# Kernel optimization log

Hardware: AMD Instinct MI355X
Metric: run time of the kernel (lower is better)

The kernel has to match this reference:

```python
import jax, jax.numpy as jnp
import numpy as np

D = 2048          # lstm_size
V = 4096          # uniform num_tokens for all 5 decision groups
NUM_LAYERS = 4    # len(num_tokens) - 1 loop iterations; one final decode after


def setup_inputs() -> dict:
    key = jax.random.key(0)
    ks = jax.random.split(key, 10)
    s = 0.02
    n = lambda k, shape: jax.random.normal(k, shape, dtype=jnp.float32) * s
    return {
        "emb0": n(ks[0], (1, D)),                 # Embedding(1, D) initial input
        "w_ih": n(ks[1], (4 * D, D)),             # LSTMCell input weights (i,f,g,o)
        "w_hh": n(ks[2], (4 * D, D)),
        "b_ih": jnp.zeros((4 * D,), jnp.float32),
        "b_hh": jnp.zeros((4 * D,), jnp.float32),
        "lin1_w": n(ks[3], (D, D)),
        "lin1_b": jnp.zeros((D,), jnp.float32),
        "lin2_w": n(ks[4], (D, D)),
        "lin2_b": jnp.zeros((D,), jnp.float32),
        "lin3_w": n(ks[5], (1, D)),
        "lin3_b": jnp.zeros((1,), jnp.float32),
        "dec_w": n(ks[6], (5, V, D)),             # 5 decoders Linear(D, V)
        "dec_b": jnp.zeros((5, V), jnp.float32),
        "emb_tables": n(ks[7], (4, V, D)),        # only embeddings[0..3] are used
    }


def _lstm_cell(x, h, c, w_ih, w_hh, b_ih, b_hh):
    # torch.nn.LSTMCell math; gate order i, f, g, o
    gates = x @ w_ih.T + b_ih + h @ w_hh.T + b_hh
    i, f, g, o = jnp.split(gates, 4, axis=-1)
    i, f, o = jax.nn.sigmoid(i), jax.nn.sigmoid(f), jax.nn.sigmoid(o)
    g = jnp.tanh(g)
    c_new = f * c + i * g
    h_new = o * jnp.tanh(c_new)
    return h_new, c_new


def reference(emb0, w_ih, w_hh, b_ih, b_hh, lin1_w, lin1_b, lin2_w, lin2_b,
              lin3_w, lin3_b, dec_w, dec_b, emb_tables):
    key = jax.random.key(42)
    step = 0

    def sample(logits, step):
        # stable softmax stats computed once via log_softmax
        logp = jax.nn.log_softmax(logits, axis=-1)
        p = jnp.exp(logp)
        ent = -(logp * p).sum(1)                              # (1,)
        idx = jax.random.categorical(jax.random.fold_in(key, step), logits, axis=-1)  # (1,)
        sel_lp = jnp.take_along_axis(logp, idx[:, None], axis=1).squeeze(1)           # (1,)
        return idx, sel_lp, jax.lax.stop_gradient(ent)

    # NOTE: source names the LSTMCell outputs (next_c, next_h) = lstm(...),
    # i.e. swapped vs torch's (h, c). State threading stays consistent, but all
    # downstream linears/decoders/all_h consume the CELL state c. Reproduced here.
    h = jnp.zeros((1, D), jnp.float32)
    c = jnp.zeros((1, D), jnp.float32)
    inputs = emb0
    all_c, all_cw = [], []
    arc, lps, ents = [], [], []

    for layer_id in range(NUM_LAYERS):
        h, c = _lstm_cell(inputs, h, c, w_ih, w_hh, b_ih, b_hh)
        all_c.append(c)
        all_cw.append(c @ lin1_w.T + lin1_b)
        query = jnp.tanh((c @ lin2_w.T + lin2_b) + jnp.concatenate(all_cw, 0))  # (layer_id+1, D)
        logits = (query @ lin3_w.T + lin3_b).reshape(1, layer_id + 1)
        skip_idx, lp, en = sample(logits, step); step += 1
        arc.append(skip_idx); lps.append(lp); ents.append(en)
        inputs = jnp.concatenate(all_c, 0)[skip_idx]            # (1, D)

        h, c = _lstm_cell(inputs, h, c, w_ih, w_hh, b_ih, b_hh)
        logits = c @ dec_w[layer_id].T + dec_b[layer_id]        # (1, V)
        func, lp, en = sample(logits, step); step += 1
        arc.append(func); lps.append(lp); ents.append(en)
        inputs = emb_tables[layer_id][func]                     # (1, D)

    # final model decision
    h, c = _lstm_cell(inputs, h, c, w_ih, w_hh, b_ih, b_hh)
    logits = c @ dec_w[-1].T + dec_b[-1]
    func, lp, en = sample(logits, step)
    arc.append(func); lps.append(lp); ents.append(en)

    arc_seq = jnp.concatenate(arc, 0)            # (9,) int32
    sample_entropy = jnp.concatenate(ents, 0)    # (9,)
    sample_log_probs = jnp.concatenate(lps, 0)   # (9,)
    return arc_seq, sample_entropy, sample_log_probs
```

## Files before the change

kernel.cpp:

```cpp
#include <hip/hip_runtime.h>
#include <stdint.h>

#define D 2048
#define V 4096
#define TINYF 1.17549435e-38f
#define NINF (-__builtin_huge_valf())

#if __has_builtin(__builtin_amdgcn_cvt_pk_f32_fp8) && __has_builtin(__builtin_amdgcn_cvt_pk_fp8_f32)
#define HWFP8 1
#define POSTSCALE 0.015625f
#else
#define HWFP8 0
#define POSTSCALE 1.52587890625e-05f
#endif

typedef float vfloat2 __attribute__((ext_vector_type(2)));
typedef float vfloat4 __attribute__((ext_vector_type(4)));

__device__ __forceinline__ void tf_block(uint32_t k0, uint32_t k1, uint32_t x0, uint32_t x1,
                                         uint32_t& o0, uint32_t& o1) {
  uint32_t ks2 = k0 ^ k1 ^ 0x1BD11BDAu;
  uint32_t ks[3] = {k0, k1, ks2};
  x0 += k0; x1 += k1;
  const uint32_t rotA[4] = {13u, 15u, 26u, 6u};
  const uint32_t rotB[4] = {17u, 29u, 16u, 24u};
#pragma unroll
  for (int i = 0; i < 5; ++i) {
    const uint32_t* rot = (i & 1) ? rotB : rotA;
#pragma unroll
    for (int j = 0; j < 4; ++j) {
      uint32_t r = rot[j];
      x0 += x1;
      x1 = (x1 << r) | (x1 >> (32u - r));
      x1 ^= x0;
    }
    x0 += ks[(i + 1) % 3];
    x1 += ks[(i + 2) % 3] + (uint32_t)(i + 1);
  }
  o0 = x0; o1 = x1;
}

__device__ __forceinline__ float gumbel_at(uint32_t k1, uint32_t k2, int i) {
  uint32_t o0, o1;
  tf_block(k1, k2, 0u, (uint32_t)i, o0, o1);
  uint32_t bits = o0 ^ o1;
  float u = __uint_as_float((bits >> 9) | 0x3F800000u) - 1.0f;
  u = fmaxf(TINYF, u + TINYF);
  return -logf(-logf(u));
}

#if !HWFP8
__device__ __forceinline__ float dec1(uint32_t v) {
  uint32_t e = (v >> 3) & 15u, m = v & 7u;
  int K = e ? (int)((8u + m) << e) : (int)(m << 1);
  float f = (float)K;
  return (v & 0x80u) ? -f : f;
}
__device__ __forceinline__ uint32_t enc1(float xf) {
  uint32_t b = __float_as_uint(xf);
  uint32_t s = (b >> 24) & 0x80u;
  float ax = fabsf(xf);
  if (ax < 0.015625f) return s | (uint32_t)(int)rintf(ax * 512.f);
  uint32_t ab = b & 0x7FFFFFFFu;
  ab += 0x7FFFFu + ((ab >> 20) & 1u);
  int e = (int)(ab >> 23) - 120;
  uint32_t m = (ab >> 20) & 7u;
  if (e < 1) return s | (uint32_t)(int)rintf(ax * 512.f);
  if (e > 15) { e = 15; m = 7u; }
  return s | ((uint32_t)e << 3) | m;
}
#endif

__device__ __forceinline__ void dec8(uint2 u, float* w) {
#if HWFP8
  vfloat2 a = __builtin_amdgcn_cvt_pk_f32_fp8((int)u.x, false);
  vfloat2 b = __builtin_amdgcn_cvt_pk_f32_fp8((int)u.x, true);
  vfloat2 c = __builtin_amdgcn_cvt_pk_f32_fp8((int)u.y, false);
  vfloat2 d = __builtin_amdgcn_cvt_pk_f32_fp8((int)u.y, true);
  w[0] = a.x; w[1] = a.y; w[2] = b.x; w[3] = b.y;
  w[4] = c.x; w[5] = c.y; w[6] = d.x; w[7] = d.y;
#else
  uint32_t p = u.x, q = u.y;
  w[0] = dec1(p & 255u); w[1] = dec1((p >> 8) & 255u);
  w[2] = dec1((p >> 16) & 255u); w[3] = dec1(p >> 24);
  w[4] = dec1(q & 255u); w[5] = dec1((q >> 8) & 255u);
  w[6] = dec1((q >> 16) & 255u); w[7] = dec1(q >> 24);
#endif
}

__device__ __forceinline__ uint2 enc8(const float* v) {
  uint2 o;
#if HWFP8
  int lo = __builtin_amdgcn_cvt_pk_fp8_f32(v[0], v[1], 0, false);
  lo     = __builtin_amdgcn_cvt_pk_fp8_f32(v[2], v[3], lo, true);
  int hi = __builtin_amdgcn_cvt_pk_fp8_f32(v[4], v[5], 0, false);
  hi     = __builtin_amdgcn_cvt_pk_fp8_f32(v[6], v[7], hi, true);
  o.x = (uint32_t)lo; o.y = (uint32_t)hi;
#else
  o.x = enc1(v[0]) | (enc1(v[1]) << 8) | (enc1(v[2]) << 16) | (enc1(v[3]) << 24);
  o.y = enc1(v[4]) | (enc1(v[5]) << 8) | (enc1(v[6]) << 16) | (enc1(v[7]) << 24);
#endif
  return o;
}

__device__ __forceinline__ float4 ntload4(const float4* p) {
  vfloat4 v = __builtin_nontemporal_load((const vfloat4*)p);
  return make_float4(v.x, v.y, v.z, v.w);
}

__device__ __forceinline__ float row_dot8(const uint8_t* __restrict__ row,
                                          const float* __restrict__ xs, int lane) {
  float a = 0.f;
#pragma unroll
  for (int k = lane * 8; k < D; k += 512) {
    uint2 u = *(const uint2*)(row + k);
    float w[8]; dec8(u, w);
    float4 x0 = *(const float4*)(xs + k);
    float4 x1 = *(const float4*)(xs + k + 4);
    a += w[0] * x0.x + w[1] * x0.y + w[2] * x0.z + w[3] * x0.w
       + w[4] * x1.x + w[5] * x1.y + w[6] * x1.z + w[7] * x1.w;
  }
  return a;
}

__device__ __forceinline__ float row_dot_conv(const float* __restrict__ row,
                                              const float* __restrict__ xs, int lane,
                                              uint8_t* __restrict__ out8) {
  float a = 0.f;
#pragma unroll
  for (int k = lane * 8; k < D; k += 512) {
    float4 w0 = ntload4((const float4*)(row + k));
    float4 w1 = ntload4((const float4*)(row + k + 4));
    float4 x0 = *(const float4*)(xs + k);
    float4 x1 = *(const float4*)(xs + k + 4);
    a += w0.x * x0.x + w0.y * x0.y + w0.z * x0.z + w0.w * x0.w
       + w1.x * x1.x + w1.y * x1.y + w1.z * x1.z + w1.w * x1.w;
    float v[8] = {w0.x * 64.f, w0.y * 64.f, w0.z * 64.f, w0.w * 64.f,
                  w1.x * 64.f, w1.y * 64.f, w1.z * 64.f, w1.w * 64.f};
    *(uint2*)(out8 + k) = enc8(v);
  }
  return a;
}

struct SampPart { float m, S, T, bv; int bi; };

__device__ __forceinline__ void merge_part(SampPart& a, float qm, float qS, float qT,
                                           float qb, int qi) {
  float nm = fmaxf(a.m, qm);
  float ea = expf(a.m - nm), eq = expf(qm - nm);
  a.T = (a.T + (a.m - nm) * a.S) * ea + (qT + (qm - nm) * qS) * eq;
  a.S = a.S * ea + qS * eq;
  a.m = nm;
  if (qb > a.bv || (qb == a.bv && qi < a.bi)) { a.bv = qb; a.bi = qi; }
}

__device__ __forceinline__ SampPart reduce_parts(const float4* __restrict__ part4,
                                                 const int* __restrict__ parti,
                                                 float* rm, float* rS, float* rT,
                                                 float* rb, int* ri, int tid) {
  float4 p = part4[4 * tid];
  SampPart a = {p.x, p.y, p.z, p.w, parti[4 * tid]};
#pragma unroll
  for (int r = 1; r < 4; ++r) {
    float4 q = part4[4 * tid + r];
    merge_part(a, q.x, q.y, q.z, q.w, parti[4 * tid + r]);
  }
  rm[tid] = a.m; rS[tid] = a.S; rT[tid] = a.T; rb[tid] = a.bv; ri[tid] = a.bi;
  __syncthreads();
  for (int st = 128; st; st >>= 1) {
    if (tid < st) {
      merge_part(a, rm[tid + st], rS[tid + st], rT[tid + st], rb[tid + st], ri[tid + st]);
      rm[tid] = a.m; rS[tid] = a.S; rT[tid] = a.T; rb[tid] = a.bv; ri[tid] = a.bi;
    }
    __syncthreads();
  }
  SampPart res = {rm[0], rS[0], rT[0], rb[0], ri[0]};
  __syncthreads();
  return res;
}

__device__ __forceinline__ void block_partial(const float* sl4, int base, int step,
                                              float4* __restrict__ part4,
                                              int* __restrict__ parti, int blk) {
  uint32_t k1, k2; tf_block(0u, 42u, 0u, (uint32_t)step, k1, k2);
  float x0 = sl4[0], x1 = sl4[1], x2 = sl4[2], x3 = sl4[3];
  float pm = fmaxf(fmaxf(x0, x1), fmaxf(x2, x3));
  float e0 = expf(x0 - pm), e1 = expf(x1 - pm), e2 = expf(x2 - pm), e3 = expf(x3 - pm);
  float pS = e0 + e1 + e2 + e3;
  float pT = e0 * (x0 - pm) + e1 * (x1 - pm) + e2 * (x2 - pm) + e3 * (x3 - pm);
  float pb = NINF; int pbi = base;
  float g;
  g = gumbel_at(k1, k2, base + 0) + x0; if (g > pb) { pb = g; pbi = base + 0; }
  g = gumbel_at(k1, k2, base + 1) + x1; if (g > pb) { pb = g; pbi = base + 1; }
  g = gumbel_at(k1, k2, base + 2) + x2; if (g > pb) { pb = g; pbi = base + 2; }
  g = gumbel_at(k1, k2, base + 3) + x3; if (g > pb) { pb = g; pbi = base + 3; }
  part4[blk] = make_float4(pm, pS, pT, pb);
  parti[blk] = pbi;
}

template <bool CONV, bool SAMPLE>
__global__ __launch_bounds__(256) void lstm_cell_k(
    const void* __restrict__ w_ih_v, const void* __restrict__ w_hh_v,
    uint8_t* __restrict__ wih8_out, uint8_t* __restrict__ whh8_out,
    const float* __restrict__ b_ih, const float* __restrict__ b_hh,
    const float* __restrict__ x_base,
    const float4* __restrict__ part4, const int* __restrict__ parti,
    const float* __restrict__ logits,
    const float* __restrict__ h_in, const float* __restrict__ c_in,
    float* __restrict__ h_out, float* __restrict__ c_out, float* __restrict__ c_copy,
    float* __restrict__ out_arc, float* __restrict__ out_ent, float* __restrict__ out_lp) {
  __shared__ float xs[D];
  __shared__ float hs[D];
  __shared__ float rm[256], rS[256], rT[256], rb[256];
  __shared__ int ri[256];
  int tid = threadIdx.x;
  const float* x = x_base;
  if (SAMPLE) {
    SampPart g = reduce_parts(part4, parti, rm, rS, rT, rb, ri, tid);
    if (tid == 0 && blockIdx.x == 0) {
      float L = logf(g.S);
      *out_arc = (float)g.bi;
      *out_ent = L - g.T / g.S;
      *out_lp  = logits[g.bi] - g.m - L;
    }
    x = x_base + (size_t)g.bi * D;
  }
  for (int i = tid; i < D; i += 256) { xs[i] = x[i]; hs[i] = h_in ? h_in[i] : 0.f; }
  __syncthreads();
  int wave = tid >> 6, lane = tid & 63;
  int j = blockIdx.x * 4 + wave;
  float gv[4];
#pragma unroll
  for (int m4 = 0; m4 < 4; ++m4) {
    size_t roff = (size_t)(m4 * D + j) * D;
    float a;
    if (CONV) {
      a = row_dot_conv((const float*)w_ih_v + roff, xs, lane, wih8_out + roff)
        + row_dot_conv((const float*)w_hh_v + roff, hs, lane, whh8_out + roff);
    } else {
      a = row_dot8((const uint8_t*)w_ih_v + roff, xs, lane)
        + row_dot8((const uint8_t*)w_hh_v + roff, hs, lane);
      a *= POSTSCALE;
    }
#pragma unroll
    for (int off = 32; off > 0; off >>= 1) a += __shfl_down(a, off, 64);
    gv[m4] = a + b_ih[m4 * D + j] + b_hh[m4 * D + j];
  }
  if (lane == 0) {
    float ig = 1.f / (1.f + expf(-gv[0]));
    float fg = 1.f / (1.f + expf(-gv[1]));
    float gg = tanhf(gv[2]);
    float og = 1.f / (1.f + expf(-gv[3]));
    float ci = c_in ? c_in[j] : 0.f;
    float cn = fg * ci + ig * gg;
    float hn = og * tanhf(cn);
    c_out[j] = cn;
    h_out[j] = hn;
    if (c_copy) c_copy[j] = cn;
  }
}

template <int NC, bool CONV>
__global__ __launch_bounds__(256) void spec_lin_k(
    const uint8_t* __restrict__ w_ih, const uint8_t* __restrict__ w_hh,
    const float* __restrict__ b_ih, const float* __restrict__ b_hh,
    const float* __restrict__ h1, const float* __restrict__ all_c,
    const void* __restrict__ l1_v, const float* __restrict__ l1b,
    const void* __restrict__ l2_v, const float* __restrict__ l2b,
    uint8_t* __restrict__ l18_out, uint8_t* __restrict__ l28_out,
    const float* __restrict__ c1,
    float* __restrict__ g_ih, float* __restrict__ g_hh,
    float* __restrict__ cw_dst, float* __restrict__ qb) {
  __shared__ float xs[D];
  int tid = threadIdx.x;
  int wave = tid >> 6, lane = tid & 63;
  int b = blockIdx.x;
  if (b < 512) {
    int j = b * 4 + wave;
    float acc[4][NC + 1];
#pragma unroll
    for (int m = 0; m < 4; ++m)
#pragma unroll
      for (int t = 0; t < NC + 1; ++t) acc[m][t] = 0.f;
    for (int k = lane * 8; k < D; k += 512) {
      float xh[8];
      float xc[NC][8];
      *(float4*)xh       = *(const float4*)(h1 + k);
      *(float4*)(xh + 4) = *(const float4*)(h1 + k + 4);
#pragma unroll
      for (int t = 0; t < NC; ++t) {
        *(float4*)(xc[t])     = *(const float4*)(all_c + (size_t)t * D + k);
        *(float4*)(xc[t] + 4) = *(const float4*)(all_c + (size_t)t * D + k + 4);
      }
#pragma unroll
      for (int m = 0; m < 4; ++m) {
        float wi[8], wh[8];
        dec8(*(const uint2*)(w_ih + (size_t)(m * D + j) * D + k), wi);
        dec8(*(const uint2*)(w_hh + (size_t)(m * D + j) * D + k), wh);
#pragma unroll
        for (int e = 0; e < 8; ++e) acc[m][0] += wh[e] * xh[e];
#pragma unroll
        for (int t = 0; t < NC; ++t)
#pragma unroll
          for (int e = 0; e < 8; ++e) acc[m][1 + t] += wi[e] * xc[t][e];
      }
    }
#pragma unroll
    for (int m = 0; m < 4; ++m)
#pragma unroll
      for (int t = 0; t < NC + 1; ++t) {
        float a = acc[m][t];
#pragma unroll
        for (int o = 32; o > 0; o >>= 1) a += __shfl_down(a, o, 64);
        if (lane == 0) {
          if (t == 0) g_hh[m * D + j] = a * POSTSCALE + b_ih[m * D + j] + b_hh[m * D + j];
          else        g_ih[((size_t)(t - 1) * 4 + m) * D + j] = a * POSTSCALE;
        }
      }
  } else {
    for (int i = tid; i < D; i += 256) xs[i] = c1[i];
    __syncthreads();
    int b2 = b - 512;
    const void* Wp; const float* bp; float* dst; uint8_t* o8; int row;
    if (b2 < 512) { row = b2 * 4 + wave; Wp = l1_v; bp = l1b; dst = cw_dst; o8 = l18_out; }
    else          { row = (b2 - 512) * 4 + wave; Wp = l2_v; bp = l2b; dst = qb; o8 = l28_out; }
    size_t roff = (size_t)row * D;
    float a;
    if (CONV) a = row_dot_conv((const float*)Wp + roff, xs, lane, o8 + roff);
    else      a = row_dot8((const uint8_t*)Wp + roff, xs, lane) * POSTSCALE;
#pragma unroll
    for (int o = 32; o > 0; o >>= 1) a += __shfl_down(a, o, 64);
    if (lane == 0) dst[row] = a + bp[row];
  }
}

__global__ __launch_bounds__(256) void dec_fused_k(
    const float* __restrict__ Wdec, const float* __restrict__ bdec,
    const float* __restrict__ g_ih, const float* __restrict__ g_hh,
    const float* __restrict__ c1,
    const float* __restrict__ qb, const float* __restrict__ all_cw,
    const float* __restrict__ lin3_w, const float* __restrict__ lin3_b,
    int ncand, int step,
    float* __restrict__ logits,
    float* __restrict__ h2_out, float* __restrict__ c2_out,
    float* __restrict__ out_arc, float* __restrict__ out_ent, float* __restrict__ out_lp,
    float4* __restrict__ part4, int* __restrict__ parti) {
  __shared__ float xs[D];
  __shared__ float red[16];
  __shared__ float sl4[4];
  __shared__ int s_sel;
  int tid = threadIdx.x, wave = tid >> 6, lane = tid & 63;
  for (int t = 0; t < ncand; ++t) {
    float s = 0.f;
    for (int k = tid; k < D; k += 256) s += tanhf(qb[k] + all_cw[(size_t)t * D + k]) * lin3_w[k];
#pragma unroll
    for (int o = 32; o > 0; o >>= 1) s += __shfl_down(s, o, 64);
    if (lane == 0) red[t * 4 + wave] = s;
  }
  __syncthreads();
  if (tid == 0) {
    float sl[4];
    for (int t = 0; t < ncand; ++t)
      sl[t] = red[t * 4] + red[t * 4 + 1] + red[t * 4 + 2] + red[t * 4 + 3] + lin3_b[0];
    uint32_t k1, k2; tf_block(0u, 42u, 0u, (uint32_t)step, k1, k2);
    float m = NINF;
    for (int i = 0; i < ncand; ++i) m = fmaxf(m, sl[i]);
    float S = 0.f, T = 0.f;
    for (int i = 0; i < ncand; ++i) { float e = expf(sl[i] - m); S += e; T += e * (sl[i] - m); }
    float L = logf(S);
    float bv = NINF; int bi = 0;
    for (int i = 0; i < ncand; ++i) {
      float sc = gumbel_at(k1, k2, i) + sl[i];
      if (sc > bv) { bv = sc; bi = i; }
    }
    s_sel = bi;
    if (blockIdx.x == 0) {
      *out_arc = (float)bi;
      *out_ent = L - T / S;
      *out_lp  = sl[bi] - m - L;
    }
  }
  __syncthreads();
  int sel = s_sel;
  const float* gi = g_ih + (size_t)sel * 4 * D;
  bool b0 = (blockIdx.x == 0);
  for (int j = tid; j < D; j += 256) {
    float gI = gi[j]         + g_hh[j];
    float gF = gi[D + j]     + g_hh[D + j];
    float gG = gi[2 * D + j] + g_hh[2 * D + j];
    float gO = gi[3 * D + j] + g_hh[3 * D + j];
    float ig = 1.f / (1.f + expf(-gI));
    float fg = 1.f / (1.f + expf(-gF));
    float gg = tanhf(gG);
    float og = 1.f / (1.f + expf(-gO));
    float cn = fg * c1[j] + ig * gg;
    xs[j] = cn;
    if (b0) { c2_out[j] = cn; h2_out[j] = og * tanhf(cn); }
  }
  __syncthreads();
  int row = blockIdx.x * 4 + wave;
  const float* wr = Wdec + (size_t)row * D;
  float a = 0.f;
#pragma unroll
  for (int k = lane * 4; k < D; k += 256) {
    float4 w = ntload4((const float4*)(wr + k));
    float4 x = *(const float4*)(xs + k);
    a += w.x * x.x + w.y * x.y + w.z * x.z + w.w * x.w;
  }
#pragma unroll
  for (int o = 32; o > 0; o >>= 1) a += __shfl_down(a, o, 64);
  if (lane == 0) { float lv = a + bdec[row]; logits[row] = lv; sl4[wave] = lv; }
  __syncthreads();
  if (tid == 0) block_partial(sl4, blockIdx.x * 4, step + 1, part4, parti, blockIdx.x);
}

__global__ __launch_bounds__(256) void gemv_k(
    const float* __restrict__ W, const float* __restrict__ bias,
    const float* __restrict__ c, float* __restrict__ y, int step,
    float4* __restrict__ part4, int* __restrict__ parti) {
  __shared__ float xs[D];
  __shared__ float sl4[4];
  int tid = threadIdx.x;
  for (int i = tid; i < D; i += 256) xs[i] = c[i];
  __syncthreads();
  int wave = tid >> 6, lane = tid & 63;
  int row = blockIdx.x * 4 + wave;
  const float* wr = W + (size_t)row * D;
  float a = 0.f;
#pragma unroll
  for (int k = lane * 4; k < D; k += 256) {
    float4 w = ntload4((const float4*)(wr + k));
    float4 x = *(const float4*)(xs + k);
    a += w.x * x.x + w.y * x.y + w.z * x.z + w.w * x.w;
  }
#pragma unroll
  for (int o = 32; o > 0; o >>= 1) a += __shfl_down(a, o, 64);
  if (lane == 0) { float lv = a + bias[row]; y[row] = lv; sl4[wave] = lv; }
  __syncthreads();
  if (tid == 0) block_partial(sl4, blockIdx.x * 4, step, part4, parti, blockIdx.x);
}

__global__ __launch_bounds__(256) void reduce_sample_k(
    const float4* __restrict__ part4, const int* __restrict__ parti,
    const float* __restrict__ logits,
    float* __restrict__ out_arc, float* __restrict__ out_ent, float* __restrict__ out_lp) {
  __shared__ float rm[256], rS[256], rT[256], rb[256];
  __shared__ int ri[256];
  int tid = threadIdx.x;
  SampPart g = reduce_parts(part4, parti, rm, rS, rT, rb, ri, tid);
  if (tid == 0) {
    float L = logf(g.S);
    *out_arc = (float)g.bi;
    *out_ent = L - g.T / g.S;
    *out_lp  = logits[g.bi] - g.m - L;
  }
}

extern "C" void kernel_launch(void* const* d_in, const int* in_sizes, int n_in,
                              void* d_out, int out_size, void* d_ws, size_t ws_size,
                              hipStream_t stream) {
  const float* emb0   = (const float*)d_in[0];
  const float* w_ih   = (const float*)d_in[1];
  const float* w_hh   = (const float*)d_in[2];
  const float* b_ih   = (const float*)d_in[3];
  const float* b_hh   = (const float*)d_in[4];
  const float* lin1_w = (const float*)d_in[5];
  const float* lin1_b = (const float*)d_in[6];
  const float* lin2_w = (const float*)d_in[7];
  const float* lin2_b = (const float*)d_in[8];
  const float* lin3_w = (const float*)d_in[9];
  const float* lin3_b = (const float*)d_in[10];
  const float* dec_w  = (const float*)d_in[11];
  const float* dec_b  = (const float*)d_in[12];
  const float* embt   = (const float*)d_in[13];

  float* out = (float*)d_out;
  float* ws = (float*)d_ws;

  float* hA     = ws;
  float* cA     = ws + D;
  float* hB     = ws + 2 * D;
  float* cB     = ws + 3 * D;
  float* all_c  = ws + 4 * D;
  float* all_cw = ws + 8 * D;
  float* qb     = ws + 12 * D;
  float* logits = ws + 13 * D;
  float* g_hh   = ws + 15 * D;
  float* g_ih   = ws + 19 * D;
  float4* part4 = (float4*)(ws + 36 * D);
  int* parti    = (int*)(ws + 38 * D);
  uint8_t* w8   = (uint8_t*)(ws + 40 * D);
  uint8_t* wih8 = w8;
  uint8_t* whh8 = w8 + (size_t)4 * D * D;
  uint8_t* l18  = w8 + (size_t)8 * D * D;
  uint8_t* l28  = w8 + (size_t)9 * D * D;

  for (int layer = 0; layer < 4; ++layer) {
    float* ccopy = all_c + (size_t)layer * D;
    if (layer == 0) {
      lstm_cell_k<true, false><<<512, 256, 0, stream>>>(
          w_ih, w_hh, wih8, whh8, b_ih, b_hh, emb0,
          nullptr, nullptr, nullptr, nullptr, nullptr,
          hA, cA, ccopy, nullptr, nullptr, nullptr);
    } else {
      int ps = 2 * layer - 1;
      lstm_cell_k<false, true><<<512, 256, 0, stream>>>(
          wih8, whh8, nullptr, nullptr, b_ih, b_hh,
          embt + (size_t)(layer - 1) * V * D,
          part4, parti, logits, hB, cB,
          hA, cA, ccopy, out + ps, out + 9 + ps, out + 18 + ps);
    }
    float* cw = all_cw + (size_t)layer * D;
    if (layer == 0) {
      spec_lin_k<1, true><<<1536, 256, 0, stream>>>(
          wih8, whh8, b_ih, b_hh, hA, all_c,
          lin1_w, lin1_b, lin2_w, lin2_b, l18, l28,
          cA, g_ih, g_hh, cw, qb);
    } else {
      switch (layer) {
        case 1:  spec_lin_k<2, false><<<1536, 256, 0, stream>>>(wih8, whh8, b_ih, b_hh, hA, all_c, l18, lin1_b, l28, lin2_b, nullptr, nullptr, cA, g_ih, g_hh, cw, qb); break;
        case 2:  spec_lin_k<3, false><<<1536, 256, 0, stream>>>(wih8, whh8, b_ih, b_hh, hA, all_c, l18, lin1_b, l28, lin2_b, nullptr, nullptr, cA, g_ih, g_hh, cw, qb); break;
        default: spec_lin_k<4, false><<<1536, 256, 0, stream>>>(wih8, whh8, b_ih, b_hh, hA, all_c, l18, lin1_b, l28, lin2_b, nullptr, nullptr, cA, g_ih, g_hh, cw, qb); break;
      }
    }
    int step = 2 * layer;
    dec_fused_k<<<V / 4, 256, 0, stream>>>(dec_w + (size_t)layer * V * D,
                                           dec_b + (size_t)layer * V,
                                           g_ih, g_hh, cA, qb, all_cw, lin3_w, lin3_b,
                                           layer + 1, step, logits, hB, cB,
                                           out + step, out + 9 + step, out + 18 + step,
                                           part4, parti);
  }

  lstm_cell_k<false, true><<<512, 256, 0, stream>>>(
      wih8, whh8, nullptr, nullptr, b_ih, b_hh,
      embt + (size_t)3 * V * D, part4, parti, logits, hB, cB,
      hA, cA, nullptr, out + 7, out + 16, out + 25);
  gemv_k<<<V / 4, 256, 0, stream>>>(dec_w + (size_t)4 * V * D, dec_b + (size_t)4 * V,
                                    cA, logits, 8, part4, parti);
  reduce_sample_k<<<1, 256, 0, stream>>>(part4, parti, logits, out + 8, out + 17, out + 26);
}
```

Baseline: 265.8 us.

## Skip zero-state W_hh in first LSTM cell, interleave gate loads, prefetch decoder rows

The first LSTM cell no longer multiplies by W_hh, since the initial hidden state is zero. The fp32-to-fp8 conversion of W_hh moves into the speculative linear kernel, which already reads that matrix. The LSTM and linear GEMV loops now interleave all four gate rows per k step, so more loads are in flight at once. The decoder and final GEMV kernels load their weight rows into registers before the dependent sampling and LSTM work, hiding memory latency behind the serial phase. The cost is higher register pressure, and the first speculative kernel now reads fp32 W_hh.

```diff
diff --git a/kernel.cpp b/kernel.cpp
--- a/kernel.cpp
+++ b/kernel.cpp
@@ -106,40 +106,6 @@
 __device__ __forceinline__ float4 ntload4(const float4* p) {
   vfloat4 v = __builtin_nontemporal_load((const vfloat4*)p);
   return make_float4(v.x, v.y, v.z, v.w);
-}
-
-__device__ __forceinline__ float row_dot8(const uint8_t* __restrict__ row,
-                                          const float* __restrict__ xs, int lane) {
-  float a = 0.f;
-#pragma unroll
-  for (int k = lane * 8; k < D; k += 512) {
-    uint2 u = *(const uint2*)(row + k);
-    float w[8]; dec8(u, w);
-    float4 x0 = *(const float4*)(xs + k);
-    float4 x1 = *(const float4*)(xs + k + 4);
-    a += w[0] * x0.x + w[1] * x0.y + w[2] * x0.z + w[3] * x0.w
-       + w[4] * x1.x + w[5] * x1.y + w[6] * x1.z + w[7] * x1.w;
-  }
-  return a;
-}
-
-__device__ __forceinline__ float row_dot_conv(const float* __restrict__ row,
-                                              const float* __restrict__ xs, int lane,
-                                              uint8_t* __restrict__ out8) {
-  float a = 0.f;
-#pragma unroll
-  for (int k = lane * 8; k < D; k += 512) {
-    float4 w0 = ntload4((const float4*)(row + k));
-    float4 w1 = ntload4((const float4*)(row + k + 4));
-    float4 x0 = *(const float4*)(xs + k);
-    float4 x1 = *(const float4*)(xs + k + 4);
-    a += w0.x * x0.x + w0.y * x0.y + w0.z * x0.z + w0.w * x0.w
-       + w1.x * x1.x + w1.y * x1.y + w1.z * x1.z + w1.w * x1.w;
-    float v[8] = {w0.x * 64.f, w0.y * 64.f, w0.z * 64.f, w0.w * 64.f,
-                  w1.x * 64.f, w1.y * 64.f, w1.z * 64.f, w1.w * 64.f};
-    *(uint2*)(out8 + k) = enc8(v);
-  }
-  return a;
 }
 
 struct SampPart { float m, S, T, bv; int bi; };
@@ -201,7 +167,7 @@
 template <bool CONV, bool SAMPLE>
 __global__ __launch_bounds__(256) void lstm_cell_k(
     const void* __restrict__ w_ih_v, const void* __restrict__ w_hh_v,
-    uint8_t* __restrict__ wih8_out, uint8_t* __restrict__ whh8_out,
+    uint8_t* __restrict__ wih8_out,
     const float* __restrict__ b_ih, const float* __restrict__ b_hh,
     const float* __restrict__ x_base,
     const float4* __restrict__ part4, const int* __restrict__ parti,
@@ -225,33 +191,60 @@
     }
     x = x_base + (size_t)g.bi * D;
   }
-  for (int i = tid; i < D; i += 256) { xs[i] = x[i]; hs[i] = h_in ? h_in[i] : 0.f; }
+  for (int i = tid; i < D; i += 256) {
+    xs[i] = x[i];
+    if (!CONV) hs[i] = h_in[i];
+  }
   __syncthreads();
   int wave = tid >> 6, lane = tid & 63;
   int j = blockIdx.x * 4 + wave;
+  float accI[4] = {0.f, 0.f, 0.f, 0.f};
+  float accH[4] = {0.f, 0.f, 0.f, 0.f};
+  for (int k = lane * 8; k < D; k += 512) {
+    float x8[8];
+    *(float4*)x8       = *(const float4*)(xs + k);
+    *(float4*)(x8 + 4) = *(const float4*)(xs + k + 4);
+    float h8[8];
+    if (!CONV) {
+      *(float4*)h8       = *(const float4*)(hs + k);
+      *(float4*)(h8 + 4) = *(const float4*)(hs + k + 4);
+    }
+#pragma unroll
+    for (int m = 0; m < 4; ++m) {
+      size_t roff = (size_t)(m * D + j) * D + k;
+      if (CONV) {
+        float4 w0 = ntload4((const float4*)((const float*)w_ih_v + roff));
+        float4 w1 = ntload4((const float4*)((const float*)w_ih_v + roff + 4));
+        accI[m] += w0.x * x8[0] + w0.y * x8[1] + w0.z * x8[2] + w0.w * x8[3]
+                 + w1.x * x8[4] + w1.y * x8[5] + w1.z * x8[6] + w1.w * x8[7];
+        float v[8] = {w0.x * 64.f, w0.y * 64.f, w0.z * 64.f, w0.w * 64.f,
+                      w1.x * 64.f, w1.y * 64.f, w1.z * 64.f, w1.w * 64.f};
+        *(uint2*)(wih8_out + roff) = enc8(v);
+      } else {
+        float wi[8], wh[8];
+        dec8(*(const uint2*)((const uint8_t*)w_ih_v + roff), wi);
+        dec8(*(const uint2*)((const uint8_t*)w_hh_v + roff), wh);
+#pragma unroll
+        for (int e = 0; e < 8; ++e) accI[m] += wi[e] * x8[e];
+#pragma unroll
+        for (int e = 0; e < 8; ++e) accH[m] += wh[e] * h8[e];
+      }
+    }
+  }
   float gv[4];
 #pragma unroll
-  for (int m4 = 0; m4 < 4; ++m4) {
-    size_t roff = (size_t)(m4 * D + j) * D;
-    float a;
-    if (CONV) {
-      a = row_dot_conv((const float*)w_ih_v + roff, xs, lane, wih8_out + roff)
-        + row_dot_conv((const float*)w_hh_v + roff, hs, lane, whh8_out + roff);
-    } else {
-      a = row_dot8((const uint8_t*)w_ih_v + roff, xs, lane)
-        + row_dot8((const uint8_t*)w_hh_v + roff, hs, lane);
-      a *= POSTSCALE;
-    }
+  for (int m = 0; m < 4; ++m) {
+    float a = CONV ? accI[m] : (accI[m] + accH[m]) * POSTSCALE;
 #pragma unroll
     for (int off = 32; off > 0; off >>= 1) a += __shfl_down(a, off, 64);
-    gv[m4] = a + b_ih[m4 * D + j] + b_hh[m4 * D + j];
+    gv[m] = a + b_ih[m * D + j] + b_hh[m * D + j];
   }
   if (lane == 0) {
     float ig = 1.f / (1.f + expf(-gv[0]));
     float fg = 1.f / (1.f + expf(-gv[1]));
     float gg = tanhf(gv[2]);
     float og = 1.f / (1.f + expf(-gv[3]));
-    float ci = c_in ? c_in[j] : 0.f;
+    float ci = CONV ? 0.f : c_in[j];
     float cn = fg * ci + ig * gg;
     float hn = og * tanhf(cn);
     c_out[j] = cn;
@@ -262,7 +255,8 @@
 
 template <int NC, bool CONV>
 __global__ __launch_bounds__(256) void spec_lin_k(
-    const uint8_t* __restrict__ w_ih, const uint8_t* __restrict__ w_hh,
+    const uint8_t* __restrict__ wih8, const void* __restrict__ whh_v,
+    uint8_t* __restrict__ whh8_out,
     const float* __restrict__ b_ih, const float* __restrict__ b_hh,
     const float* __restrict__ h1, const float* __restrict__ all_c,
     const void* __restrict__ l1_v, const float* __restrict__ l1b,
@@ -294,9 +288,20 @@
       }
 #pragma unroll
       for (int m = 0; m < 4; ++m) {
+        size_t roff = (size_t)(m * D + j) * D + k;
         float wi[8], wh[8];
-        dec8(*(const uint2*)(w_ih + (size_t)(m * D + j) * D + k), wi);
-        dec8(*(const uint2*)(w_hh + (size_t)(m * D + j) * D + k), wh);
+        dec8(*(const uint2*)(wih8 + roff), wi);
+        if (CONV) {
+          float4 w0 = ntload4((const float4*)((const float*)whh_v + roff));
+          float4 w1 = ntload4((const float4*)((const float*)whh_v + roff + 4));
+          wh[0] = w0.x; wh[1] = w0.y; wh[2] = w0.z; wh[3] = w0.w;
+          wh[4] = w1.x; wh[5] = w1.y; wh[6] = w1.z; wh[7] = w1.w;
+          float v[8] = {w0.x * 64.f, w0.y * 64.f, w0.z * 64.f, w0.w * 64.f,
+                        w1.x * 64.f, w1.y * 64.f, w1.z * 64.f, w1.w * 64.f};
+          *(uint2*)(whh8_out + roff) = enc8(v);
+        } else {
+          dec8(*(const uint2*)((const uint8_t*)whh_v + roff), wh);
+        }
 #pragma unroll
         for (int e = 0; e < 8; ++e) acc[m][0] += wh[e] * xh[e];
 #pragma unroll
@@ -313,8 +318,12 @@
 #pragma unroll
         for (int o = 32; o > 0; o >>= 1) a += __shfl_down(a, o, 64);
         if (lane == 0) {
-          if (t == 0) g_hh[m * D + j] = a * POSTSCALE + b_ih[m * D + j] + b_hh[m * D + j];
-          else        g_ih[((size_t)(t - 1) * 4 + m) * D + j] = a * POSTSCALE;
+          if (t == 0) {
+            float sc = CONV ? 1.f : POSTSCALE;
+            g_hh[m * D + j] = a * sc + b_ih[m * D + j] + b_hh[m * D + j];
+          } else {
+            g_ih[((size_t)(t - 1) * 4 + m) * D + j] = a * POSTSCALE;
+          }
         }
       }
   } else {
@@ -324,10 +333,28 @@
     const void* Wp; const float* bp; float* dst; uint8_t* o8; int row;
     if (b2 < 512) { row = b2 * 4 + wave; Wp = l1_v; bp = l1b; dst = cw_dst; o8 = l18_out; }
     else          { row = (b2 - 512) * 4 + wave; Wp = l2_v; bp = l2b; dst = qb; o8 = l28_out; }
-    size_t roff = (size_t)row * D;
-    float a;
-    if (CONV) a = row_dot_conv((const float*)Wp + roff, xs, lane, o8 + roff);
-    else      a = row_dot8((const uint8_t*)Wp + roff, xs, lane) * POSTSCALE;
+    size_t rbase = (size_t)row * D;
+    float a = 0.f;
+    for (int k = lane * 8; k < D; k += 512) {
+      float x0[8];
+      *(float4*)x0       = *(const float4*)(xs + k);
+      *(float4*)(x0 + 4) = *(const float4*)(xs + k + 4);
+      if (CONV) {
+        float4 w0 = ntload4((const float4*)((const float*)Wp + rbase + k));
+        float4 w1 = ntload4((const float4*)((const float*)Wp + rbase + k + 4));
+        a += w0.x * x0[0] + w0.y * x0[1] + w0.z * x0[2] + w0.w * x0[3]
+           + w1.x * x0[4] + w1.y * x0[5] + w1.z * x0[6] + w1.w * x0[7];
+        float v[8] = {w0.x * 64.f, w0.y * 64.f, w0.z * 64.f, w0.w * 64.f,
+                      w1.x * 64.f, w1.y * 64.f, w1.z * 64.f, w1.w * 64.f};
+        *(uint2*)(o8 + rbase + k) = enc8(v);
+      } else {
+        float w[8];
+        dec8(*(const uint2*)((const uint8_t*)Wp + rbase + k), w);
+#pragma unroll
+        for (int e = 0; e < 8; ++e) a += w[e] * x0[e];
+      }
+    }
+    if (!CONV) a *= POSTSCALE;
 #pragma unroll
     for (int o = 32; o > 0; o >>= 1) a += __shfl_down(a, o, 64);
     if (lane == 0) dst[row] = a + bp[row];
@@ -350,6 +377,12 @@
   __shared__ float sl4[4];
   __shared__ int s_sel;
   int tid = threadIdx.x, wave = tid >> 6, lane = tid & 63;
+  int row = blockIdx.x * 4 + wave;
+  const float* wr = Wdec + (size_t)row * D;
+  float4 wreg[8];
+#pragma unroll
+  for (int kk = 0; kk < 8; ++kk)
+    wreg[kk] = ntload4((const float4*)(wr + lane * 4 + kk * 256));
   for (int t = 0; t < ncand; ++t) {
     float s = 0.f;
     for (int k = tid; k < D; k += 256) s += tanhf(qb[k] + all_cw[(size_t)t * D + k]) * lin3_w[k];
@@ -398,14 +431,11 @@
     if (b0) { c2_out[j] = cn; h2_out[j] = og * tanhf(cn); }
   }
   __syncthreads();
-  int row = blockIdx.x * 4 + wave;
-  const float* wr = Wdec + (size_t)row * D;
   float a = 0.f;
 #pragma unroll
-  for (int k = lane * 4; k < D; k += 256) {
-    float4 w = ntload4((const float4*)(wr + k));
-    float4 x = *(const float4*)(xs + k);
-    a += w.x * x.x + w.y * x.y + w.z * x.z + w.w * x.w;
+  for (int kk = 0; kk < 8; ++kk) {
+    float4 x = *(const float4*)(xs + lane * 4 + kk * 256);
+    a += wreg[kk].x * x.x + wreg[kk].y * x.y + wreg[kk].z * x.z + wreg[kk].w * x.w;
   }
 #pragma unroll
   for (int o = 32; o > 0; o >>= 1) a += __shfl_down(a, o, 64);
@@ -420,18 +450,20 @@
     float4* __restrict__ part4, int* __restrict__ parti) {
   __shared__ float xs[D];
   __shared__ float sl4[4];
-  int tid = threadIdx.x;
-  for (int i = tid; i < D; i += 256) xs[i] = c[i];
-  __syncthreads();
-  int wave = tid >> 6, lane = tid & 63;
+  int tid = threadIdx.x, wave = tid >> 6, lane = tid & 63;
   int row = blockIdx.x * 4 + wave;
   const float* wr = W + (size_t)row * D;
+  float4 wreg[8];
+#pragma unroll
+  for (int kk = 0; kk < 8; ++kk)
+    wreg[kk] = ntload4((const float4*)(wr + lane * 4 + kk * 256));
+  for (int i = tid; i < D; i += 256) xs[i] = c[i];
+  __syncthreads();
   float a = 0.f;
 #pragma unroll
-  for (int k = lane * 4; k < D; k += 256) {
-    float4 w = ntload4((const float4*)(wr + k));
-    float4 x = *(const float4*)(xs + k);
-    a += w.x * x.x + w.y * x.y + w.z * x.z + w.w * x.w;
+  for (int kk = 0; kk < 8; ++kk) {
+    float4 x = *(const float4*)(xs + lane * 4 + kk * 256);
+    a += wreg[kk].x * x.x + wreg[kk].y * x.y + wreg[kk].z * x.z + wreg[kk].w * x.w;
   }
 #pragma unroll
   for (int o = 32; o > 0; o >>= 1) a += __shfl_down(a, o, 64);
@@ -499,13 +531,13 @@
     float* ccopy = all_c + (size_t)layer * D;
     if (layer == 0) {
       lstm_cell_k<true, false><<<512, 256, 0, stream>>>(
-          w_ih, w_hh, wih8, whh8, b_ih, b_hh, emb0,
+          w_ih, nullptr, wih8, b_ih, b_hh, emb0,
           nullptr, nullptr, nullptr, nullptr, nullptr,
           hA, cA, ccopy, nullptr, nullptr, nullptr);
     } else {
       int ps = 2 * layer - 1;
       lstm_cell_k<false, true><<<512, 256, 0, stream>>>(
-          wih8, whh8, nullptr, nullptr, b_ih, b_hh,
+          wih8, whh8, nullptr, b_ih, b_hh,
           embt + (size_t)(layer - 1) * V * D,
           part4, parti, logits, hB, cB,
           hA, cA, ccopy, out + ps, out + 9 + ps, out + 18 + ps);
@@ -513,14 +545,14 @@
     float* cw = all_cw + (size_t)layer * D;
     if (layer == 0) {
       spec_lin_k<1, true><<<1536, 256, 0, stream>>>(
-          wih8, whh8, b_ih, b_hh, hA, all_c,
+          wih8, w_hh, whh8, b_ih, b_hh, hA, all_c,
           lin1_w, lin1_b, lin2_w, lin2_b, l18, l28,
           cA, g_ih, g_hh, cw, qb);
     } else {
       switch (layer) {
-        case 1:  spec_lin_k<2, false><<<1536, 256, 0, stream>>>(wih8, whh8, b_ih, b_hh, hA, all_c, l18, lin1_b, l28, lin2_b, nullptr, nullptr, cA, g_ih, g_hh, cw, qb); break;
-        case 2:  spec_lin_k<3, false><<<1536, 256, 0, stream>>>(wih8, whh8, b_ih, b_hh, hA, all_c, l18, lin1_b, l28, lin2_b, nullptr, nullptr, cA, g_ih, g_hh, cw, qb); break;
-        default: spec_lin_k<4, false><<<1536, 256, 0, stream>>>(wih8, whh8, b_ih, b_hh, hA, all_c, l18, lin1_b, l28, lin2_b, nullptr, nullptr, cA, g_ih, g_hh, cw, qb); break;
+        case 1:  spec_lin_k<2, false><<<1536, 256, 0, stream>>>(wih8, whh8, nullptr, b_ih, b_hh, hA, all_c, l18, lin1_b, l28, lin2_b, nullptr, nullptr, cA, g_ih, g_hh, cw, qb); break;
+        case 2:  spec_lin_k<3, false><<<1536, 256, 0, stream>>>(wih8, whh8, nullptr, b_ih, b_hh, hA, all_c, l18, lin1_b, l28, lin2_b, nullptr, nullptr, cA, g_ih, g_hh, cw, qb); break;
+        default: spec_lin_k<4, false><<<1536, 256, 0, stream>>>(wih8, whh8, nullptr, b_ih, b_hh, hA, all_c, l18, lin1_b, l28, lin2_b, nullptr, nullptr, cA, g_ih, g_hh, cw, qb); break;
       }
     }
     int step = 2 * layer;
@@ -533,7 +565,7 @@
   }
 
   lstm_cell_k<false, true><<<512, 256, 0, stream>>>(
-      wih8, whh8, nullptr, nullptr, b_ih, b_hh,
+      wih8, whh8, nullptr, b_ih, b_hh,
       embt + (size_t)3 * V * D, part4, parti, logits, hB, cB,
       hA, cA, nullptr, out + 7, out + 16, out + 25);
   gemv_k<<<V / 4, 256, 0, stream>>>(dec_w + (size_t)4 * V * D, dec_b + (size_t)4 * V,
```

Result: slower. 271.6 us (+2.2%).

## Split LSTM cell work so each block owns one hidden unit across four gate waves

Applied to the files above, without the earlier changes.

The LSTM cell kernel now launches one block per hidden unit (2048 blocks), with each of the four waves computing one gate row. Previously each wave computed all four gate rows serially across 512 blocks. The gate results are combined through shared memory before thread 0 applies the cell update. The sampling reduction scratch now aliases the xs shared buffer to cut shared memory use, and the fp8 dot product is inlined with separate ih/hh accumulators. Each block still redundantly reduces the sampling partials and loads x/h into shared memory, so that per-block overhead is now paid four times as often.

```diff
diff --git a/kernel.cpp b/kernel.cpp
--- a/kernel.cpp
+++ b/kernel.cpp
@@ -211,11 +211,15 @@
     float* __restrict__ out_arc, float* __restrict__ out_ent, float* __restrict__ out_lp) {
   __shared__ float xs[D];
   __shared__ float hs[D];
-  __shared__ float rm[256], rS[256], rT[256], rb[256];
-  __shared__ int ri[256];
+  __shared__ float sgv[4];
   int tid = threadIdx.x;
   const float* x = x_base;
   if (SAMPLE) {
+    float* rm = xs;
+    float* rS = xs + 256;
+    float* rT = xs + 512;
+    float* rb = xs + 768;
+    int*   ri = (int*)(xs + 1024);
     SampPart g = reduce_parts(part4, parti, rm, rS, rT, rb, ri, tid);
     if (tid == 0 && blockIdx.x == 0) {
       float L = logf(g.S);
@@ -225,32 +229,50 @@
     }
     x = x_base + (size_t)g.bi * D;
   }
-  for (int i = tid; i < D; i += 256) { xs[i] = x[i]; hs[i] = h_in ? h_in[i] : 0.f; }
+  for (int i = tid; i < D; i += 256) {
+    xs[i] = x[i];
+    hs[i] = h_in ? h_in[i] : 0.f;
+  }
   __syncthreads();
   int wave = tid >> 6, lane = tid & 63;
-  int j = blockIdx.x * 4 + wave;
-  float gv[4];
-#pragma unroll
-  for (int m4 = 0; m4 < 4; ++m4) {
-    size_t roff = (size_t)(m4 * D + j) * D;
-    float a;
-    if (CONV) {
-      a = row_dot_conv((const float*)w_ih_v + roff, xs, lane, wih8_out + roff)
-        + row_dot_conv((const float*)w_hh_v + roff, hs, lane, whh8_out + roff);
-    } else {
-      a = row_dot8((const uint8_t*)w_ih_v + roff, xs, lane)
-        + row_dot8((const uint8_t*)w_hh_v + roff, hs, lane);
-      a *= POSTSCALE;
-    }
-#pragma unroll
-    for (int off = 32; off > 0; off >>= 1) a += __shfl_down(a, off, 64);
-    gv[m4] = a + b_ih[m4 * D + j] + b_hh[m4 * D + j];
-  }
-  if (lane == 0) {
-    float ig = 1.f / (1.f + expf(-gv[0]));
-    float fg = 1.f / (1.f + expf(-gv[1]));
-    float gg = tanhf(gv[2]);
-    float og = 1.f / (1.f + expf(-gv[3]));
+  int j = blockIdx.x;
+  int m = wave;
+  size_t roff = (size_t)(m * D + j) * D;
+  float a;
+  if (CONV) {
+    a = row_dot_conv((const float*)w_ih_v + roff, xs, lane, wih8_out + roff)
+      + row_dot_conv((const float*)w_hh_v + roff, hs, lane, whh8_out + roff);
+  } else {
+    const uint8_t* ri8 = (const uint8_t*)w_ih_v + roff;
+    const uint8_t* rh8 = (const uint8_t*)w_hh_v + roff;
+    float accI = 0.f, accH = 0.f;
+#pragma unroll
+    for (int k = lane * 8; k < D; k += 512) {
+      uint2 ui = *(const uint2*)(ri8 + k);
+      uint2 uh = *(const uint2*)(rh8 + k);
+      float wi[8], wh[8];
+      dec8(ui, wi);
+      dec8(uh, wh);
+      float4 x0 = *(const float4*)(xs + k);
+      float4 x1 = *(const float4*)(xs + k + 4);
+      float4 h0 = *(const float4*)(hs + k);
+      float4 h1 = *(const float4*)(hs + k + 4);
+      accI += wi[0] * x0.x + wi[1] * x0.y + wi[2] * x0.z + wi[3] * x0.w
+            + wi[4] * x1.x + wi[5] * x1.y + wi[6] * x1.z + wi[7] * x1.w;
+      accH += wh[0] * h0.x + wh[1] * h0.y + wh[2] * h0.z + wh[3] * h0.w
+            + wh[4] * h1.x + wh[5] * h1.y + wh[6] * h1.z + wh[7] * h1.w;
+    }
+    a = (accI + accH) * POSTSCALE;
+  }
+#pragma unroll
+  for (int off = 32; off > 0; off >>= 1) a += __shfl_down(a, off, 64);
+  if (lane == 0) sgv[m] = a + b_ih[m * D + j] + b_hh[m * D + j];
+  __syncthreads();
+  if (tid == 0) {
+    float ig = 1.f / (1.f + expf(-sgv[0]));
+    float fg = 1.f / (1.f + expf(-sgv[1]));
+    float gg = tanhf(sgv[2]);
+    float og = 1.f / (1.f + expf(-sgv[3]));
     float ci = c_in ? c_in[j] : 0.f;
     float cn = fg * ci + ig * gg;
     float hn = og * tanhf(cn);
@@ -294,9 +316,10 @@
       }
 #pragma unroll
       for (int m = 0; m < 4; ++m) {
+        size_t roff = (size_t)(m * D + j) * D + k;
         float wi[8], wh[8];
-        dec8(*(const uint2*)(w_ih + (size_t)(m * D + j) * D + k), wi);
-        dec8(*(const uint2*)(w_hh + (size_t)(m * D + j) * D + k), wh);
+        dec8(*(const uint2*)(w_ih + roff), wi);
+        dec8(*(const uint2*)(w_hh + roff), wh);
 #pragma unroll
         for (int e = 0; e < 8; ++e) acc[m][0] += wh[e] * xh[e];
 #pragma unroll
@@ -498,13 +521,13 @@
   for (int layer = 0; layer < 4; ++layer) {
     float* ccopy = all_c + (size_t)layer * D;
     if (layer == 0) {
-      lstm_cell_k<true, false><<<512, 256, 0, stream>>>(
+      lstm_cell_k<true, false><<<2048, 256, 0, stream>>>(
           w_ih, w_hh, wih8, whh8, b_ih, b_hh, emb0,
           nullptr, nullptr, nullptr, nullptr, nullptr,
           hA, cA, ccopy, nullptr, nullptr, nullptr);
     } else {
       int ps = 2 * layer - 1;
-      lstm_cell_k<false, true><<<512, 256, 0, stream>>>(
+      lstm_cell_k<false, true><<<2048, 256, 0, stream>>>(
           wih8, whh8, nullptr, nullptr, b_ih, b_hh,
           embt + (size_t)(layer - 1) * V * D,
           part4, parti, logits, hB, cB,
@@ -532,7 +555,7 @@
                                            part4, parti);
   }
 
-  lstm_cell_k<false, true><<<512, 256, 0, stream>>>(
+  lstm_cell_k<false, true><<<2048, 256, 0, stream>>>(
       wih8, whh8, nullptr, nullptr, b_ih, b_hh,
       embt + (size_t)3 * V * D, part4, parti, logits, hB, cB,
       hA, cA, nullptr, out + 7, out + 16, out + 25);
```

Result: slower. 284.3 us (+7.0%).
